# Optimization experiments

Hardware: AMD Instinct MI355X
Metric: run time of the kernel (lower is better)

## Reference

```python
import jax, jax.numpy as jnp
import numpy as np

B_SZ, L, D, N = 4, 2048, 768, 16


def setup_inputs() -> dict:
    key = jax.random.key(0)
    ks = jax.random.split(key, 8)
    x = jax.random.normal(ks[0], (B_SZ, L, D), dtype=jnp.float32)
    # A_log initialized as log(arange(1..N)) repeated over d, as in the module
    A_log = jnp.log(jnp.broadcast_to(jnp.arange(1, N + 1, dtype=jnp.float32), (D, N)))
    # s_b_c: Linear(D, 2N)
    W_bc = jax.random.normal(ks[1], (2 * N, D), dtype=jnp.float32) / jnp.sqrt(D)
    b_bc = jnp.zeros((2 * N,), dtype=jnp.float32)
    # s_1: Linear(D, 1)
    W_1 = jax.random.normal(ks[2], (1, D), dtype=jnp.float32) / jnp.sqrt(D)
    b_1 = jnp.zeros((1,), dtype=jnp.float32)
    # s_delta: Linear(1, D)
    W_d = jax.random.normal(ks[3], (D, 1), dtype=jnp.float32)
    b_d = jnp.zeros((D,), dtype=jnp.float32)
    return {"x": x, "A_log": A_log, "W_bc": W_bc, "b_bc": b_bc,
            "W_1": W_1, "b_1": b_1, "W_d": W_d, "b_d": b_d}


def reference(x, A_log, W_bc, b_bc, W_1, b_1, W_d, b_d):
    b, l, d = x.shape
    n = A_log.shape[1]
    A = -jnp.exp(A_log)                                   # (d, n)
    BandC = x @ W_bc.T + b_bc                             # (b, l, 2n)
    Bm, Cm = BandC[..., :n], BandC[..., n:]               # (b, l, n) each
    # delta = softplus(s_delta(s_1(x)))  -> (b, l, d)
    s1 = x @ W_1.T + b_1                                  # (b, l, 1)
    delta = jax.nn.softplus(s1 @ W_d.T + b_d)             # (b, l, d)
    deltaA = jnp.exp(jnp.einsum('bld,dn->bldn', delta, A))        # (b, l, d, n)
    deltaB_u = jnp.einsum('bld,bln,bld->bldn', delta, Bm, x)      # (b, l, d, n)

    # sequential selective-scan over time with lax.scan
    dA_t = jnp.moveaxis(deltaA, 1, 0)      # (l, b, d, n)
    dBu_t = jnp.moveaxis(deltaB_u, 1, 0)   # (l, b, d, n)
    C_t = jnp.moveaxis(Cm, 1, 0)           # (l, b, n)

    def step(h, inp):
        dA_i, dBu_i, c_i = inp
        h = dA_i * h + dBu_i               # (b, d, n)
        y = jnp.einsum('bdn,bn->bd', h, c_i)
        return h, y

    h0 = jnp.zeros((b, d, n), dtype=x.dtype)
    _, ys = jax.lax.scan(step, h0, (dA_t, dBu_t, C_t))
    return jnp.moveaxis(ys, 0, 1)          # (b, l, d)
```

## Files before the change

### kernel.cpp

```cpp
#include <hip/hip_runtime.h>

#define L_SEQ 2048
#define D_DIM 768
#define N_ST 16
#define NB 4
#define NJ 33
#define NROWS (NB * L_SEQ)
#define PROJ_ELEMS (NROWS * NJ)

#define DSPLIT 8
#define DSEG (D_DIM / DSPLIT)
#define DK 32
#define NCHUNK (DSEG / DK)
#define RB 128
#define XST 132
#define WST 64

__device__ __forceinline__ float fast_exp2(float x) {
#if __has_builtin(__builtin_amdgcn_exp2f)
  return __builtin_amdgcn_exp2f(x);
#else
  return __expf(x * 0.69314718055994531f);
#endif
}

__device__ __forceinline__ float softplus_f(float v) {
  float e = __expf(v);
  float l = __logf(1.0f + e);
  return (v > 15.0f) ? v : l;
}

__global__ __launch_bounds__(256) void k_proj_gemm(
    const float* __restrict__ x, const float* __restrict__ W_bc,
    const float* __restrict__ W_1, float* __restrict__ PBC) {
  __shared__ float xs_t[DK * XST];
  __shared__ float ws_t[DK * WST];

  const int ds  = blockIdx.x % DSPLIT;
  const int rb0 = (blockIdx.x / DSPLIT) * RB;
  const int dbase = ds * DSEG;
  const int tid = threadIdx.x;

  const int rg = tid & 31;
  const int jg = tid >> 5;

  float acc[4][5];
#pragma unroll
  for (int i = 0; i < 4; ++i)
#pragma unroll
    for (int k = 0; k < 5; ++k) acc[i][k] = 0.0f;

  const int lrow = tid >> 1;
  const int lhalf = (tid & 1) * 16;
  const float* xg_row = x + (size_t)(rb0 + lrow) * D_DIM + dbase + lhalf;

  for (int ch = 0; ch < NCHUNK; ++ch) {
    const int dc = dbase + ch * DK;
    float4 xv[4];
#pragma unroll
    for (int q = 0; q < 4; ++q)
      xv[q] = *(const float4*)(xg_row + ch * DK + q * 4);
    float wv[8];
    int widx[8];
#pragma unroll
    for (int u = 0; u < 8; ++u) {
      int idx = tid + u * 256;
      int dk = idx >> 6, slot = idx & 63;
      int wjg = slot >> 3, wk = slot & 7;
      int j = wjg + 8 * wk;
      float v = 0.0f;
      if (wk < 5) {
        if (j < 32)       v = W_bc[(size_t)j * D_DIM + dc + dk];
        else if (j == 32) v = W_1[dc + dk];
      }
      wv[u] = v; widx[u] = dk * WST + slot;
    }
    __syncthreads();
#pragma unroll
    for (int q = 0; q < 4; ++q) {
      xs_t[(lhalf + q * 4 + 0) * XST + lrow] = xv[q].x;
      xs_t[(lhalf + q * 4 + 1) * XST + lrow] = xv[q].y;
      xs_t[(lhalf + q * 4 + 2) * XST + lrow] = xv[q].z;
      xs_t[(lhalf + q * 4 + 3) * XST + lrow] = xv[q].w;
    }
#pragma unroll
    for (int u = 0; u < 8; ++u) ws_t[widx[u]] = wv[u];
    __syncthreads();
#pragma unroll 8
    for (int dk = 0; dk < DK; ++dk) {
      float4 xr = *(const float4*)&xs_t[dk * XST + rg * 4];
      float4 wr = *(const float4*)&ws_t[dk * WST + jg * 8];
      float w4  = ws_t[dk * WST + jg * 8 + 4];
      float xa[4] = {xr.x, xr.y, xr.z, xr.w};
      float wa[5] = {wr.x, wr.y, wr.z, wr.w, w4};
#pragma unroll
      for (int i = 0; i < 4; ++i)
#pragma unroll
        for (int k = 0; k < 5; ++k)
          acc[i][k] = fmaf(xa[i], wa[k], acc[i][k]);
    }
  }

  float* pb = PBC + (size_t)ds * PROJ_ELEMS;
#pragma unroll
  for (int i = 0; i < 4; ++i) {
    int row = rb0 + rg * 4 + i;
#pragma unroll
    for (int k = 0; k < 5; ++k) {
      int j = jg + 8 * k;
      if (k < 4 || jg == 0) pb[(size_t)row * NJ + j] = acc[i][k];
    }
  }
}

__global__ __launch_bounds__(256) void k_proj_reduce(
    const float* __restrict__ PBC, const float* __restrict__ b_bc,
    const float* __restrict__ b_1, float* __restrict__ BC33) {
  const int idx = blockIdx.x * 256 + threadIdx.x;
  const int j = idx % NJ;
  float s = 0.0f;
#pragma unroll
  for (int k = 0; k < DSPLIT; ++k) s += PBC[(size_t)k * PROJ_ELEMS + idx];
  s += (j < 32) ? b_bc[j] : b_1[0];
  BC33[idx] = s;
}

template <int LC>
__global__ __launch_bounds__(256) void k_scan1(
    const float* __restrict__ x, const float* __restrict__ A_log,
    const float* __restrict__ W_d, const float* __restrict__ b_d,
    const float* __restrict__ BC33, float* __restrict__ DS,
    float* __restrict__ H, int NC) {
  const int cb = blockIdx.x % 3;
  const int c  = (blockIdx.x / 3) % NC;
  const int b  = blockIdx.x / (3 * NC);
  const int d  = cb * 256 + threadIdx.x;

  const float wd = W_d[d], bd = b_d[d];
  float Aln[N_ST];
#pragma unroll
  for (int n = 0; n < N_ST; ++n)
    Aln[n] = -__expf(A_log[d * N_ST + n]) * 1.44269504088896f;

  float h[N_ST];
#pragma unroll
  for (int n = 0; n < N_ST; ++n) h[n] = 0.0f;
  float dsum = 0.0f;

  const int l0 = c * LC;
  const float* bc = BC33 + (size_t)(b * L_SEQ + l0) * NJ;
  const float* xp = x + (size_t)(b * L_SEQ + l0) * D_DIM + d;

#pragma unroll 8
  for (int l = 0; l < LC; ++l) {
    float s1 = bc[l * NJ + 32];
    float delta = softplus_f(fmaf(s1, wd, bd));
    float xv = xp[(size_t)l * D_DIM];
    float f = delta * xv;
    dsum += delta;
#pragma unroll
    for (int n = 0; n < N_ST; ++n) {
      float dA = fast_exp2(delta * Aln[n]);
      h[n] = fmaf(dA, h[n], f * bc[l * NJ + n]);
    }
  }

  DS[((size_t)b * NC + c) * D_DIM + d] = dsum;
  size_t base = ((size_t)(b * NC + c) * D_DIM + d) * N_ST;
  float4* H4 = (float4*)(H + base);
#pragma unroll
  for (int q = 0; q < 4; ++q)
    H4[q] = make_float4(h[4*q], h[4*q+1], h[4*q+2], h[4*q+3]);
}

__global__ __launch_bounds__(256) void k_combine(
    const float* __restrict__ A_log, const float* __restrict__ DS,
    float* __restrict__ H, int NC) {
  const int b  = blockIdx.x / 48;
  const int tl = (blockIdx.x % 48) * 256 + threadIdx.x;
  const int d = tl >> 4, n = tl & 15;
  const float Aln = -__expf(A_log[d * N_ST + n]) * 1.44269504088896f;

  const float* dsp = DS + (size_t)b * NC * D_DIM + d;
  float* Hp = H + (size_t)b * NC * (D_DIM * N_ST) + tl;

  float h = 0.0f;
  float ds_c = dsp[0];
  float hold = Hp[0];
#pragma unroll 4
  for (int c = 0; c < NC; ++c) {
    float ds_n = 0.0f, hold_n = 0.0f;
    if (c + 1 < NC) {
      ds_n   = dsp[(size_t)(c + 1) * D_DIM];
      hold_n = Hp[(size_t)(c + 1) * (D_DIM * N_ST)];
    }
    float p = fast_exp2(Aln * ds_c);
    Hp[(size_t)c * (D_DIM * N_ST)] = h;
    h = fmaf(p, h, hold);
    ds_c = ds_n; hold = hold_n;
  }
}

template <int LC>
__global__ __launch_bounds__(256) void k_scan2(
    const float* __restrict__ x, const float* __restrict__ A_log,
    const float* __restrict__ W_d, const float* __restrict__ b_d,
    const float* __restrict__ BC33, const float* __restrict__ HIN,
    float* __restrict__ out, int NC) {
  const int cb = blockIdx.x % 3;
  const int c  = (blockIdx.x / 3) % NC;
  const int b  = blockIdx.x / (3 * NC);
  const int d  = cb * 256 + threadIdx.x;

  const float wd = W_d[d], bd = b_d[d];
  float Aln[N_ST];
#pragma unroll
  for (int n = 0; n < N_ST; ++n)
    Aln[n] = -__expf(A_log[d * N_ST + n]) * 1.44269504088896f;

  float h[N_ST];
  size_t base = ((size_t)(b * NC + c) * D_DIM + d) * N_ST;
  const float4* HIN4 = (const float4*)(HIN + base);
#pragma unroll
  for (int q = 0; q < 4; ++q) {
    float4 v = HIN4[q];
    h[4*q] = v.x; h[4*q+1] = v.y; h[4*q+2] = v.z; h[4*q+3] = v.w;
  }

  const int l0 = c * LC;
  const float* bc = BC33 + (size_t)(b * L_SEQ + l0) * NJ;
  const float* xp = x + (size_t)(b * L_SEQ + l0) * D_DIM + d;
  float* op = out + (size_t)(b * L_SEQ + l0) * D_DIM + d;

#pragma unroll 8
  for (int l = 0; l < LC; ++l) {
    float s1 = bc[l * NJ + 32];
    float delta = softplus_f(fmaf(s1, wd, bd));
    float xv = xp[(size_t)l * D_DIM];
    float f = delta * xv;
    float y = 0.0f;
#pragma unroll
    for (int n = 0; n < N_ST; ++n) {
      float dA = fast_exp2(delta * Aln[n]);
      h[n] = fmaf(dA, h[n], f * bc[l * NJ + n]);
      y = fmaf(h[n], bc[l * NJ + 16 + n], y);
    }
    op[(size_t)l * D_DIM] = y;
  }
}

extern "C" void kernel_launch(void* const* d_in, const int* in_sizes, int n_in,
                              void* d_out, int out_size, void* d_ws, size_t ws_size,
                              hipStream_t stream) {
  const float* x     = (const float*)d_in[0];
  const float* A_log = (const float*)d_in[1];
  const float* W_bc  = (const float*)d_in[2];
  const float* b_bc  = (const float*)d_in[3];
  const float* W_1   = (const float*)d_in[4];
  const float* b_1   = (const float*)d_in[5];
  const float* W_d   = (const float*)d_in[6];
  const float* b_d   = (const float*)d_in[7];
  float* out = (float*)d_out;
  float* ws  = (float*)d_ws;

  int NC = 8;
  const int cands[4] = {128, 64, 32, 16};
  for (int i = 0; i < 4; ++i) {
    size_t need = (9ull * PROJ_ELEMS + (3072ull + 49152ull) * cands[i]) * 4ull;
    if (ws_size >= need) { NC = cands[i]; break; }
  }

  float* BC33 = ws;
  float* PBC  = ws + PROJ_ELEMS;
  float* DSb  = PBC + (size_t)DSPLIT * PROJ_ELEMS;
  float* H    = DSb + (size_t)3072 * NC;

  k_proj_gemm<<<(NROWS / RB) * DSPLIT, 256, 0, stream>>>(x, W_bc, W_1, PBC);
  k_proj_reduce<<<PROJ_ELEMS / 256, 256, 0, stream>>>(PBC, b_bc, b_1, BC33);

  const int gs = 3 * NB * NC;
  switch (NC) {
    case 128:
      k_scan1<16><<<gs, 256, 0, stream>>>(x, A_log, W_d, b_d, BC33, DSb, H, NC);
      k_combine<<<192, 256, 0, stream>>>(A_log, DSb, H, NC);
      k_scan2<16><<<gs, 256, 0, stream>>>(x, A_log, W_d, b_d, BC33, H, out, NC);
      break;
    case 64:
      k_scan1<32><<<gs, 256, 0, stream>>>(x, A_log, W_d, b_d, BC33, DSb, H, NC);
      k_combine<<<192, 256, 0, stream>>>(A_log, DSb, H, NC);
      k_scan2<32><<<gs, 256, 0, stream>>>(x, A_log, W_d, b_d, BC33, H, out, NC);
      break;
    case 32:
      k_scan1<64><<<gs, 256, 0, stream>>>(x, A_log, W_d, b_d, BC33, DSb, H, NC);
      k_combine<<<192, 256, 0, stream>>>(A_log, DSb, H, NC);
      k_scan2<64><<<gs, 256, 0, stream>>>(x, A_log, W_d, b_d, BC33, H, out, NC);
      break;
    case 16:
      k_scan1<128><<<gs, 256, 0, stream>>>(x, A_log, W_d, b_d, BC33, DSb, H, NC);
      k_combine<<<192, 256, 0, stream>>>(A_log, DSb, H, NC);
      k_scan2<128><<<gs, 256, 0, stream>>>(x, A_log, W_d, b_d, BC33, H, out, NC);
      break;
    default:
      k_scan1<256><<<gs, 256, 0, stream>>>(x, A_log, W_d, b_d, BC33, DSb, H, NC);
      k_combine<<<192, 256, 0, stream>>>(A_log, DSb, H, NC);
      k_scan2<256><<<gs, 256, 0, stream>>>(x, A_log, W_d, b_d, BC33, H, out, NC);
      break;
  }
}
```

Baseline: 179.4 us.

## Fuse three-pass chunked scan into single-pass decoupled look-back scan

```diff
diff --git a/kernel.cpp b/kernel.cpp
--- a/kernel.cpp
+++ b/kernel.cpp
@@ -7,6 +7,7 @@
 #define NJ 33
 #define NROWS (NB * L_SEQ)
 #define PROJ_ELEMS (NROWS * NJ)
+#define NCHAIN (NB * 3)
 
 #define DSPLIT 8
 #define DSEG (D_DIM / DSPLIT)
@@ -126,15 +127,19 @@
 }
 
 template <int LC>
-__global__ __launch_bounds__(256) void k_scan1(
+__global__ __launch_bounds__(256) void k_scan_fused(
     const float* __restrict__ x, const float* __restrict__ A_log,
     const float* __restrict__ W_d, const float* __restrict__ b_d,
-    const float* __restrict__ BC33, float* __restrict__ DS,
-    float* __restrict__ H, int NC) {
-  const int cb = blockIdx.x % 3;
-  const int c  = (blockIdx.x / 3) % NC;
-  const int b  = blockIdx.x / (3 * NC);
-  const int d  = cb * 256 + threadIdx.x;
+    const float* __restrict__ BC33, float* __restrict__ AGG_DS,
+    float* __restrict__ AGG_H, float* __restrict__ AGG_HO,
+    int* flags, float* __restrict__ out) {
+  __shared__ float ylds[LC * 256];
+  const int tid = threadIdx.x;
+  const int bid = blockIdx.x;
+  const int chain = bid % NCHAIN;
+  const int c = bid / NCHAIN;
+  const int b = chain / 3, cb = chain % 3;
+  const int d = cb * 256 + tid;
 
   const float wd = W_d[d], bd = b_d[d];
   float Aln[N_ST];
@@ -158,86 +163,6 @@
     float xv = xp[(size_t)l * D_DIM];
     float f = delta * xv;
     dsum += delta;
-#pragma unroll
-    for (int n = 0; n < N_ST; ++n) {
-      float dA = fast_exp2(delta * Aln[n]);
-      h[n] = fmaf(dA, h[n], f * bc[l * NJ + n]);
-    }
-  }
-
-  DS[((size_t)b * NC + c) * D_DIM + d] = dsum;
-  size_t base = ((size_t)(b * NC + c) * D_DIM + d) * N_ST;
-  float4* H4 = (float4*)(H + base);
-#pragma unroll
-  for (int q = 0; q < 4; ++q)
-    H4[q] = make_float4(h[4*q], h[4*q+1], h[4*q+2], h[4*q+3]);
-}
-
-__global__ __launch_bounds__(256) void k_combine(
-    const float* __restrict__ A_log, const float* __restrict__ DS,
-    float* __restrict__ H, int NC) {
-  const int b  = blockIdx.x / 48;
-  const int tl = (blockIdx.x % 48) * 256 + threadIdx.x;
-  const int d = tl >> 4, n = tl & 15;
-  const float Aln = -__expf(A_log[d * N_ST + n]) * 1.44269504088896f;
-
-  const float* dsp = DS + (size_t)b * NC * D_DIM + d;
-  float* Hp = H + (size_t)b * NC * (D_DIM * N_ST) + tl;
-
-  float h = 0.0f;
-  float ds_c = dsp[0];
-  float hold = Hp[0];
-#pragma unroll 4
-  for (int c = 0; c < NC; ++c) {
-    float ds_n = 0.0f, hold_n = 0.0f;
-    if (c + 1 < NC) {
-      ds_n   = dsp[(size_t)(c + 1) * D_DIM];
-      hold_n = Hp[(size_t)(c + 1) * (D_DIM * N_ST)];
-    }
-    float p = fast_exp2(Aln * ds_c);
-    Hp[(size_t)c * (D_DIM * N_ST)] = h;
-    h = fmaf(p, h, hold);
-    ds_c = ds_n; hold = hold_n;
-  }
-}
-
-template <int LC>
-__global__ __launch_bounds__(256) void k_scan2(
-    const float* __restrict__ x, const float* __restrict__ A_log,
-    const float* __restrict__ W_d, const float* __restrict__ b_d,
-    const float* __restrict__ BC33, const float* __restrict__ HIN,
-    float* __restrict__ out, int NC) {
-  const int cb = blockIdx.x % 3;
-  const int c  = (blockIdx.x / 3) % NC;
-  const int b  = blockIdx.x / (3 * NC);
-  const int d  = cb * 256 + threadIdx.x;
-
-  const float wd = W_d[d], bd = b_d[d];
-  float Aln[N_ST];
-#pragma unroll
-  for (int n = 0; n < N_ST; ++n)
-    Aln[n] = -__expf(A_log[d * N_ST + n]) * 1.44269504088896f;
-
-  float h[N_ST];
-  size_t base = ((size_t)(b * NC + c) * D_DIM + d) * N_ST;
-  const float4* HIN4 = (const float4*)(HIN + base);
-#pragma unroll
-  for (int q = 0; q < 4; ++q) {
-    float4 v = HIN4[q];
-    h[4*q] = v.x; h[4*q+1] = v.y; h[4*q+2] = v.z; h[4*q+3] = v.w;
-  }
-
-  const int l0 = c * LC;
-  const float* bc = BC33 + (size_t)(b * L_SEQ + l0) * NJ;
-  const float* xp = x + (size_t)(b * L_SEQ + l0) * D_DIM + d;
-  float* op = out + (size_t)(b * L_SEQ + l0) * D_DIM + d;
-
-#pragma unroll 8
-  for (int l = 0; l < LC; ++l) {
-    float s1 = bc[l * NJ + 32];
-    float delta = softplus_f(fmaf(s1, wd, bd));
-    float xv = xp[(size_t)l * D_DIM];
-    float f = delta * xv;
     float y = 0.0f;
 #pragma unroll
     for (int n = 0; n < N_ST; ++n) {
@@ -245,7 +170,106 @@
       h[n] = fmaf(dA, h[n], f * bc[l * NJ + n]);
       y = fmaf(h[n], bc[l * NJ + 16 + n], y);
     }
-    op[(size_t)l * D_DIM] = y;
+    ylds[l * 256 + tid] = y;
+  }
+
+  const size_t pme = (size_t)bid * 256 + tid;
+  AGG_DS[pme] = dsum;
+  {
+    float4* Hme = (float4*)(AGG_H + pme * N_ST);
+#pragma unroll
+    for (int q = 0; q < 4; ++q)
+      Hme[q] = make_float4(h[4*q], h[4*q+1], h[4*q+2], h[4*q+3]);
+  }
+  __threadfence();
+  __syncthreads();
+  if (tid == 0)
+    __hip_atomic_store(flags + bid, 1, __ATOMIC_RELEASE, __HIP_MEMORY_SCOPE_AGENT);
+
+  float hin[N_ST];
+#pragma unroll
+  for (int n = 0; n < N_ST; ++n) hin[n] = 0.0f;
+  if (c > 0) {
+    float Hacc[N_ST];
+#pragma unroll
+    for (int n = 0; n < N_ST; ++n) Hacc[n] = 0.0f;
+    float dsacc = 0.0f;
+    int j = bid - NCHAIN;
+    for (;;) {
+      int f;
+      do {
+        f = __hip_atomic_load(flags + j, __ATOMIC_ACQUIRE, __HIP_MEMORY_SCOPE_AGENT);
+        if (f == 0) __builtin_amdgcn_s_sleep(2);
+      } while (f == 0);
+      const size_t pj = (size_t)j * 256 + tid;
+      if (f == 2) {
+        const float4* HO4 = (const float4*)(AGG_HO + pj * N_ST);
+        float ho[N_ST];
+#pragma unroll
+        for (int q = 0; q < 4; ++q) {
+          float4 v = HO4[q];
+          ho[4*q] = v.x; ho[4*q+1] = v.y; ho[4*q+2] = v.z; ho[4*q+3] = v.w;
+        }
+#pragma unroll
+        for (int n = 0; n < N_ST; ++n)
+          hin[n] = fmaf(fast_exp2(Aln[n] * dsacc), ho[n], Hacc[n]);
+        break;
+      } else {
+        float dsj = AGG_DS[pj];
+        const float4* HJ4 = (const float4*)(AGG_H + pj * N_ST);
+        float hj[N_ST];
+#pragma unroll
+        for (int q = 0; q < 4; ++q) {
+          float4 v = HJ4[q];
+          hj[4*q] = v.x; hj[4*q+1] = v.y; hj[4*q+2] = v.z; hj[4*q+3] = v.w;
+        }
+#pragma unroll
+        for (int n = 0; n < N_ST; ++n)
+          Hacc[n] = fmaf(fast_exp2(Aln[n] * dsacc), hj[n], Hacc[n]);
+        dsacc += dsj;
+        if (j < NCHAIN) {
+#pragma unroll
+          for (int n = 0; n < N_ST; ++n) hin[n] = Hacc[n];
+          break;
+        }
+        j -= NCHAIN;
+      }
+    }
+  }
+
+  {
+    float ho[N_ST];
+#pragma unroll
+    for (int n = 0; n < N_ST; ++n)
+      ho[n] = fmaf(fast_exp2(Aln[n] * dsum), hin[n], h[n]);
+    float4* HOme = (float4*)(AGG_HO + pme * N_ST);
+#pragma unroll
+    for (int q = 0; q < 4; ++q)
+      HOme[q] = make_float4(ho[4*q], ho[4*q+1], ho[4*q+2], ho[4*q+3]);
+  }
+  __threadfence();
+  __syncthreads();
+  if (tid == 0)
+    __hip_atomic_store(flags + bid, 2, __ATOMIC_RELEASE, __HIP_MEMORY_SCOPE_AGENT);
+
+  float* op = out + (size_t)(b * L_SEQ + l0) * D_DIM + d;
+  if (c == 0) {
+#pragma unroll 8
+    for (int l = 0; l < LC; ++l)
+      op[(size_t)l * D_DIM] = ylds[l * 256 + tid];
+  } else {
+    float S = 0.0f;
+#pragma unroll 4
+    for (int l = 0; l < LC; ++l) {
+      float s1 = bc[l * NJ + 32];
+      float delta = softplus_f(fmaf(s1, wd, bd));
+      S += delta;
+      float corr = 0.0f;
+#pragma unroll
+      for (int n = 0; n < N_ST; ++n)
+        corr = fmaf(fast_exp2(Aln[n] * S) * hin[n], bc[l * NJ + 16 + n], corr);
+      op[(size_t)l * D_DIM] = ylds[l * 256 + tid] + corr;
+    }
   }
 }
 
@@ -263,47 +287,32 @@
   float* out = (float*)d_out;
   float* ws  = (float*)d_ws;
 
-  int NC = 8;
-  const int cands[4] = {128, 64, 32, 16};
-  for (int i = 0; i < 4; ++i) {
-    size_t need = (9ull * PROJ_ELEMS + (3072ull + 49152ull) * cands[i]) * 4ull;
-    if (ws_size >= need) { NC = cands[i]; break; }
-  }
-
-  float* BC33 = ws;
-  float* PBC  = ws + PROJ_ELEMS;
-  float* DSb  = PBC + (size_t)DSPLIT * PROJ_ELEMS;
-  float* H    = DSb + (size_t)3072 * NC;
-
+  int NC = 64;
+  {
+    size_t need = (9ull * PROJ_ELEMS +
+                   (size_t)NCHAIN * 64 * 256 * (1 + 16 + 16) +
+                   (size_t)NCHAIN * 64) * 4ull;
+    if (ws_size < need) NC = 32;
+  }
+  const int nblk = NCHAIN * NC;
+  const size_t agg_cols = (size_t)nblk * 256;
+
+  float* BC33   = ws;
+  float* PBC    = BC33 + PROJ_ELEMS;
+  float* AGG_DS = PBC + (size_t)DSPLIT * PROJ_ELEMS;
+  float* AGG_H  = AGG_DS + agg_cols;
+  float* AGG_HO = AGG_H + agg_cols * N_ST;
+  int*   flags  = (int*)(AGG_HO + agg_cols * N_ST);
+
+  hipMemsetAsync(flags, 0, (size_t)nblk * sizeof(int), stream);
   k_proj_gemm<<<(NROWS / RB) * DSPLIT, 256, 0, stream>>>(x, W_bc, W_1, PBC);
   k_proj_reduce<<<PROJ_ELEMS / 256, 256, 0, stream>>>(PBC, b_bc, b_1, BC33);
 
-  const int gs = 3 * NB * NC;
-  switch (NC) {
-    case 128:
-      k_scan1<16><<<gs, 256, 0, stream>>>(x, A_log, W_d, b_d, BC33, DSb, H, NC);
-      k_combine<<<192, 256, 0, stream>>>(A_log, DSb, H, NC);
-      k_scan2<16><<<gs, 256, 0, stream>>>(x, A_log, W_d, b_d, BC33, H, out, NC);
-      break;
-    case 64:
-      k_scan1<32><<<gs, 256, 0, stream>>>(x, A_log, W_d, b_d, BC33, DSb, H, NC);
-      k_combine<<<192, 256, 0, stream>>>(A_log, DSb, H, NC);
-      k_scan2<32><<<gs, 256, 0, stream>>>(x, A_log, W_d, b_d, BC33, H, out, NC);
-      break;
-    case 32:
-      k_scan1<64><<<gs, 256, 0, stream>>>(x, A_log, W_d, b_d, BC33, DSb, H, NC);
-      k_combine<<<192, 256, 0, stream>>>(A_log, DSb, H, NC);
-      k_scan2<64><<<gs, 256, 0, stream>>>(x, A_log, W_d, b_d, BC33, H, out, NC);
-      break;
-    case 16:
-      k_scan1<128><<<gs, 256, 0, stream>>>(x, A_log, W_d, b_d, BC33, DSb, H, NC);
-      k_combine<<<192, 256, 0, stream>>>(A_log, DSb, H, NC);
-      k_scan2<128><<<gs, 256, 0, stream>>>(x, A_log, W_d, b_d, BC33, H, out, NC);
-      break;
-    default:
-      k_scan1<256><<<gs, 256, 0, stream>>>(x, A_log, W_d, b_d, BC33, DSb, H, NC);
-      k_combine<<<192, 256, 0, stream>>>(A_log, DSb, H, NC);
-      k_scan2<256><<<gs, 256, 0, stream>>>(x, A_log, W_d, b_d, BC33, H, out, NC);
-      break;
-  }
-}
+  if (NC == 64) {
+    k_scan_fused<32><<<nblk, 256, 0, stream>>>(
+        x, A_log, W_d, b_d, BC33, AGG_DS, AGG_H, AGG_HO, flags, out);
+  } else {
+    k_scan_fused<64><<<nblk, 256, 0, stream>>>(
+        x, A_log, W_d, b_d, BC33, AGG_DS, AGG_H, AGG_HO, flags, out);
+  }
+}
```

Result: slower. 644.5 us (+259.2%).
